# Optimization experiments

Measured on AMD Instinct MI355X. Metric: run time of the kernel, lower is better.

The kernel has to match this reference:

```python
import jax, jax.numpy as jnp
import numpy as np

TAU = 2.0
V_TH = 1.0
ATAN_ALPHA = 2.0
LN_EPS = 1e-5

# Surrogate-gradient spike: forward = Heaviside(v - v_th), backward = ATan surrogate
@jax.custom_vjp
def atan_spike(x):
    return (x >= 0.0).astype(x.dtype)

def _atan_spike_fwd(x):
    return atan_spike(x), x

def _atan_spike_bwd(x, g):
    grad = ATAN_ALPHA / (2.0 * (1.0 + (jnp.pi / 2.0 * ATAN_ALPHA * x) ** 2))
    return (g * grad,)

atan_spike.defvjp(_atan_spike_fwd, _atan_spike_bwd)

def layernorm(x, g, b):
    m = jnp.mean(x, axis=-1, keepdims=True)
    v = jnp.mean((x - m) ** 2, axis=-1, keepdims=True)
    return (x - m) * jax.lax.rsqrt(v + LN_EPS) * g + b

def lif_multistep(x_btd):
    """spikingjelly LIFNode: decay_input=True, v_reset=0.0 (hard reset), detach_reset=True.
    x_btd: [B, T, D]; scan over T with membrane state [B, D]; returns spikes [B, T, D]."""
    x_tbd = jnp.swapaxes(x_btd, 0, 1)  # [T, B, D]
    def step(v, xt):
        h = v + (xt - v) / TAU                      # charge (decay_input, v_reset=0)
        s = atan_spike(h - V_TH)                    # fire
        v_new = h * (1.0 - jax.lax.stop_gradient(s))  # hard reset to 0, detached spike
        return v_new, s
    _, spikes = jax.lax.scan(step, jnp.zeros_like(x_tbd[0]), x_tbd)
    return jnp.swapaxes(spikes, 0, 1)  # [B, T, D]

def setup_inputs() -> dict:
    key = jax.random.key(0)
    ks = jax.random.split(key, 3)
    B, T, D, H = 256, 256, 128, 256
    x = jax.random.normal(ks[0], (B, T, D), dtype=jnp.float32)
    W1 = jax.random.normal(ks[1], (H, D), dtype=jnp.float32) * (1.0 / np.sqrt(D))
    b1 = jnp.zeros((H,), jnp.float32)
    g1 = jnp.ones((H,), jnp.float32)
    be1 = jnp.zeros((H,), jnp.float32)
    W2 = jax.random.normal(ks[2], (D, H), dtype=jnp.float32) * (1.0 / np.sqrt(H))
    b2 = jnp.zeros((D,), jnp.float32)
    g2 = jnp.ones((D,), jnp.float32)
    be2 = jnp.zeros((D,), jnp.float32)
    return {"x": x, "W1": W1, "b1": b1, "g1": g1, "be1": be1,
            "W2": W2, "b2": b2, "g2": g2, "be2": be2}

def reference(x, W1, b1, g1, be1, W2, b2, g2, be2):
    residual = x
    h = jnp.einsum("btd,hd->bth", x, W1) + b1
    h = layernorm(h, g1, be1)
    h = lif_multistep(h)            # dropout is identity at eval
    o = jnp.einsum("bth,dh->btd", h, W2) + b2
    o = layernorm(o, g2, be2)
    o = lif_multistep(o)
    return residual + o
```

## Files before the change

kernel.cpp:

```cpp
#include <hip/hip_runtime.h>
#include <hip/hip_bf16.h>
#include <stdint.h>

#define B_ 256
#define T_ 256
#define D_ 128
#define H_ 256
#define LN_EPS 1e-5

typedef double f64x4 __attribute__((ext_vector_type(4)));

__device__ __forceinline__ bool probe_f64_mfma_layout(int l16, int lg, int* rowp)
{
  const f64x4 zz = {0.0, 0.0, 0.0, 0.0};
  const double pa_r = (lg == 0) ? (double)l16 : 0.0;
  const double pb_1 = (lg == 0) ? 1.0 : 0.0;
  const f64x4 prow = __builtin_amdgcn_mfma_f64_16x16x4f64(pa_r, pb_1, zz, 0, 0, 0);
  const double pa_1 = (lg == 0) ? 1.0 : 0.0;
  const double pb_c = (lg == 0) ? (double)l16 : 0.0;
  const f64x4 pcol = __builtin_amdgcn_mfma_f64_16x16x4f64(pa_1, pb_c, zz, 0, 0, 0);
  bool ok = true;
  int rm = 0, rp = 0;
  #pragma unroll
  for (int r = 0; r < 4; ++r) {
    const int ri = (int)prow[r];
    const int ci = (int)pcol[r];
    rowp[r] = ri;
    ok = ok && ((double)ri == prow[r]) && (ri >= 0) && (ri < 16);
    ok = ok && ((double)ci == pcol[r]) && (ci == l16);
    rm |= 1 << ri;
    rp |= ri << (4 * r);
  }
  ok = ok && (__popc(rm) == 4);
  #pragma unroll
  for (int m = 1; m <= 8; m <<= 1)
    ok = ok && (__shfl_xor(rp, m, 64) == rp);
  int rmw = rm;
  rmw |= __shfl_xor(rmw, 16, 64);
  rmw |= __shfl_xor(rmw, 32, 64);
  ok = ok && (rmw == 0xFFFF);
  return __all((int)ok) != 0;
}

__global__ __launch_bounds__(256, 2) void k1_gemm_ln(
    const float* __restrict__ x, const float* __restrict__ W1,
    const float* __restrict__ b1, const float* __restrict__ g1, const float* __restrict__ be1,
    double* __restrict__ h1, int row0)
{
  __shared__ double As[16 * 66];
  __shared__ double Bs[16 * 258];
  const int tid  = threadIdx.x;
  const int lane = tid & 63, wave = tid >> 6;
  const int l16  = lane & 15, lg = lane >> 4;
  const int orow = blockIdx.x * 64;
  const int grow = row0 + orow;
  const int wrow = wave * 16;

  int rowp[4];
  const bool ok = probe_f64_mfma_layout(l16, lg, rowp);

  auto stage = [&](int kt) {
    __syncthreads();
    {
      const int row = tid >> 2, ko = (tid & 3) * 4;
      const float4 f = *(const float4*)(x + (size_t)(grow + row) * 128 + kt + ko);
      As[(ko+0)*66 + row] = (double)f.x;
      As[(ko+1)*66 + row] = (double)f.y;
      As[(ko+2)*66 + row] = (double)f.z;
      As[(ko+3)*66 + row] = (double)f.w;
    }
    {
      const float* src = W1 + (size_t)tid * 128 + kt;
      #pragma unroll
      for (int j = 0; j < 4; ++j) {
        const float4 f = *(const float4*)(src + j * 4);
        Bs[(j*4+0)*258 + tid] = (double)f.x;
        Bs[(j*4+1)*258 + tid] = (double)f.y;
        Bs[(j*4+2)*258 + tid] = (double)f.z;
        Bs[(j*4+3)*258 + tid] = (double)f.w;
      }
    }
    __syncthreads();
  };

  if (ok) {
    f64x4 acc[16];
    #pragma unroll
    for (int ct = 0; ct < 16; ++ct) acc[ct] = (f64x4){0.0, 0.0, 0.0, 0.0};
    for (int kt = 0; kt < 128; kt += 16) {
      stage(kt);
      #pragma unroll
      for (int ks = 0; ks < 4; ++ks) {
        const int k = ks * 4 + lg;
        const double a = As[k*66 + wrow + l16];
        #pragma unroll
        for (int ct = 0; ct < 16; ++ct) {
          const double b = Bs[k*258 + ct*16 + l16];
          acc[ct] = __builtin_amdgcn_mfma_f64_16x16x4f64(a, b, acc[ct], 0, 0, 0);
        }
      }
    }
    double bb[16];
    #pragma unroll
    for (int ct = 0; ct < 16; ++ct) bb[ct] = (double)b1[ct*16 + l16];
    #pragma unroll
    for (int r = 0; r < 4; ++r) {
      double s = 0.0, q = 0.0;
      #pragma unroll
      for (int ct = 0; ct < 16; ++ct) {
        const double v = acc[ct][r] + bb[ct];
        s += v; q += v * v;
      }
      s += __shfl_xor(s, 1, 64); q += __shfl_xor(q, 1, 64);
      s += __shfl_xor(s, 2, 64); q += __shfl_xor(q, 2, 64);
      s += __shfl_xor(s, 4, 64); q += __shfl_xor(q, 4, 64);
      s += __shfl_xor(s, 8, 64); q += __shfl_xor(q, 8, 64);
      const double mean = s * (1.0/256.0);
      const double var  = q * (1.0/256.0) - mean*mean;
      const double rstd = 1.0 / sqrt(var + LN_EPS);
      const int row = orow + wrow + rowp[r];
      #pragma unroll
      for (int ct = 0; ct < 16; ++ct) {
        const int col = ct*16 + l16;
        const double v = acc[ct][r] + bb[ct];
        h1[(size_t)row*256 + col] = (v - mean) * rstd * (double)g1[col] + (double)be1[col];
      }
    }
  } else {
    double accv[64];
    #pragma unroll
    for (int c = 0; c < 64; ++c) accv[c] = 0.0;
    for (int kt = 0; kt < 128; kt += 16) {
      stage(kt);
      for (int k = 0; k < 16; ++k) {
        const double a = As[k*66 + wrow + l16];
        #pragma unroll
        for (int c = 0; c < 64; ++c)
          accv[c] = fma(a, Bs[k*258 + lg*64 + c], accv[c]);
      }
    }
    double s = 0.0, q = 0.0;
    #pragma unroll
    for (int c = 0; c < 64; ++c) {
      accv[c] += (double)b1[lg*64 + c];
      s += accv[c]; q += accv[c]*accv[c];
    }
    s += __shfl_xor(s, 16, 64); q += __shfl_xor(q, 16, 64);
    s += __shfl_xor(s, 32, 64); q += __shfl_xor(q, 32, 64);
    const double mean = s * (1.0/256.0);
    const double var  = q * (1.0/256.0) - mean*mean;
    const double rstd = 1.0 / sqrt(var + LN_EPS);
    const int row = orow + wrow + l16;
    #pragma unroll
    for (int c = 0; c < 64; ++c) {
      const int col = lg*64 + c;
      h1[(size_t)row*256 + col] = (accv[c] - mean) * rstd * (double)g1[col] + (double)be1[col];
    }
  }
}

__global__ __launch_bounds__(256) void k2_lif(
    const double* __restrict__ h1, uint8_t* __restrict__ s1)
{
  const int ci = blockIdx.x * 256 + threadIdx.x;
  const int b = ci >> 8, h = ci & 255;
  const double* p = h1 + (size_t)b * (T_*H_) + h;
  uint8_t* qp = s1 + (size_t)b * (T_*H_) + h;
  double v = 0.0;
  #pragma unroll 8
  for (int t = 0; t < T_; ++t) {
    const double xv = p[(size_t)t * H_];
    const double hm = v + (xv - v) * 0.5;
    const bool s = (hm >= 1.0);
    v = s ? 0.0 : hm;
    qp[(size_t)t * H_] = s ? (uint8_t)1 : (uint8_t)0;
  }
}

__global__ __launch_bounds__(256, 2) void k3_gemm_ln(
    const uint8_t* __restrict__ s1, const float* __restrict__ W2,
    const float* __restrict__ b2, const float* __restrict__ g2, const float* __restrict__ be2,
    double* __restrict__ h2)
{
  __shared__ double As[16 * 66];
  __shared__ double Bs[16 * 130];
  const int tid  = threadIdx.x;
  const int lane = tid & 63, wave = tid >> 6;
  const int l16  = lane & 15, lg = lane >> 4;
  const int orow = blockIdx.x * 64;
  const int wrow = wave * 16;

  int rowp[4];
  const bool ok = probe_f64_mfma_layout(l16, lg, rowp);

  auto stage = [&](int kt) {
    __syncthreads();
    {
      const int row = tid >> 2, ko = (tid & 3) * 4;
      const uint32_t u = *(const uint32_t*)(s1 + (size_t)(orow + row) * 256 + kt + ko);
      As[(ko+0)*66 + row] = (double)( u        & 0xffu);
      As[(ko+1)*66 + row] = (double)((u >> 8)  & 0xffu);
      As[(ko+2)*66 + row] = (double)((u >> 16) & 0xffu);
      As[(ko+3)*66 + row] = (double)((u >> 24) & 0xffu);
    }
    {
      const int col = tid >> 1, k0 = (tid & 1) * 8;
      const float* src = W2 + (size_t)col * 256 + kt + k0;
      #pragma unroll
      for (int j = 0; j < 2; ++j) {
        const float4 f = *(const float4*)(src + j * 4);
        Bs[(k0+j*4+0)*130 + col] = (double)f.x;
        Bs[(k0+j*4+1)*130 + col] = (double)f.y;
        Bs[(k0+j*4+2)*130 + col] = (double)f.z;
        Bs[(k0+j*4+3)*130 + col] = (double)f.w;
      }
    }
    __syncthreads();
  };

  if (ok) {
    f64x4 acc[8];
    #pragma unroll
    for (int ct = 0; ct < 8; ++ct) acc[ct] = (f64x4){0.0, 0.0, 0.0, 0.0};
    for (int kt = 0; kt < 256; kt += 16) {
      stage(kt);
      #pragma unroll
      for (int ks = 0; ks < 4; ++ks) {
        const int k = ks * 4 + lg;
        const double a = As[k*66 + wrow + l16];
        #pragma unroll
        for (int ct = 0; ct < 8; ++ct) {
          const double b = Bs[k*130 + ct*16 + l16];
          acc[ct] = __builtin_amdgcn_mfma_f64_16x16x4f64(a, b, acc[ct], 0, 0, 0);
        }
      }
    }
    double bb[8];
    #pragma unroll
    for (int ct = 0; ct < 8; ++ct) bb[ct] = (double)b2[ct*16 + l16];
    #pragma unroll
    for (int r = 0; r < 4; ++r) {
      double s = 0.0, q = 0.0;
      #pragma unroll
      for (int ct = 0; ct < 8; ++ct) {
        const double v = acc[ct][r] + bb[ct];
        s += v; q += v * v;
      }
      s += __shfl_xor(s, 1, 64); q += __shfl_xor(q, 1, 64);
      s += __shfl_xor(s, 2, 64); q += __shfl_xor(q, 2, 64);
      s += __shfl_xor(s, 4, 64); q += __shfl_xor(q, 4, 64);
      s += __shfl_xor(s, 8, 64); q += __shfl_xor(q, 8, 64);
      const double mean = s * (1.0/128.0);
      const double var  = q * (1.0/128.0) - mean*mean;
      const double rstd = 1.0 / sqrt(var + LN_EPS);
      const int row = orow + wrow + rowp[r];
      #pragma unroll
      for (int ct = 0; ct < 8; ++ct) {
        const int col = ct*16 + l16;
        const double v = acc[ct][r] + bb[ct];
        h2[(size_t)row*128 + col] = (v - mean) * rstd * (double)g2[col] + (double)be2[col];
      }
    }
  } else {
    double accv[32];
    #pragma unroll
    for (int c = 0; c < 32; ++c) accv[c] = 0.0;
    for (int kt = 0; kt < 256; kt += 16) {
      stage(kt);
      for (int k = 0; k < 16; ++k) {
        const double a = As[k*66 + wrow + l16];
        #pragma unroll
        for (int c = 0; c < 32; ++c)
          accv[c] = fma(a, Bs[k*130 + lg*32 + c], accv[c]);
      }
    }
    double s = 0.0, q = 0.0;
    #pragma unroll
    for (int c = 0; c < 32; ++c) {
      accv[c] += (double)b2[lg*32 + c];
      s += accv[c]; q += accv[c]*accv[c];
    }
    s += __shfl_xor(s, 16, 64); q += __shfl_xor(q, 16, 64);
    s += __shfl_xor(s, 32, 64); q += __shfl_xor(q, 32, 64);
    const double mean = s * (1.0/128.0);
    const double var  = q * (1.0/128.0) - mean*mean;
    const double rstd = 1.0 / sqrt(var + LN_EPS);
    const int row = orow + wrow + l16;
    #pragma unroll
    for (int c = 0; c < 32; ++c) {
      const int col = lg*32 + c;
      h2[(size_t)row*128 + col] = (accv[c] - mean) * rstd * (double)g2[col] + (double)be2[col];
    }
  }
}

__global__ __launch_bounds__(64) void k4_lif_res(
    const double* __restrict__ h2, const float* __restrict__ x,
    float* __restrict__ out, int row0)
{
  const int ci = blockIdx.x * 64 + threadIdx.x;
  const int b = ci >> 7, d = ci & 127;
  const double* p = h2 + (size_t)b * (T_*D_) + d;
  const size_t gbase = ((size_t)row0 + (size_t)b * T_) * D_ + d;
  double v = 0.0;
  #pragma unroll 8
  for (int t = 0; t < T_; ++t) {
    const double hv = p[(size_t)t * D_];
    const double hm = v + (hv - v) * 0.5;
    const bool s = (hm >= 1.0);
    v = s ? 0.0 : hm;
    out[gbase + (size_t)t * D_] = x[gbase + (size_t)t * D_] + (s ? 1.0f : 0.0f);
  }
}

extern "C" void kernel_launch(void* const* d_in, const int* in_sizes, int n_in,
                              void* d_out, int out_size, void* d_ws, size_t ws_size,
                              hipStream_t stream)
{
  const float* x   = (const float*)d_in[0];
  const float* W1  = (const float*)d_in[1];
  const float* b1  = (const float*)d_in[2];
  const float* g1  = (const float*)d_in[3];
  const float* be1 = (const float*)d_in[4];
  const float* W2  = (const float*)d_in[5];
  const float* b2  = (const float*)d_in[6];
  const float* g2  = (const float*)d_in[7];
  const float* be2 = (const float*)d_in[8];
  float* out = (float*)d_out;

  const size_t per_b = (size_t)T_*H_*sizeof(double) + (size_t)T_*H_ + (size_t)T_*D_*sizeof(double);
  int Bc = B_;
  while (Bc > 1 && (size_t)Bc * per_b > ws_size) Bc >>= 1;

  double*  h1 = (double*)d_ws;
  uint8_t* s1 = (uint8_t*)d_ws + (size_t)Bc*T_*H_*sizeof(double);
  double*  h2 = (double*)((uint8_t*)d_ws + (size_t)Bc*T_*H_*sizeof(double) + (size_t)Bc*T_*H_);

  const int nchunk = B_ / Bc;
  for (int c = 0; c < nchunk; ++c) {
    const int row0 = c * Bc * T_;
    k1_gemm_ln<<<dim3(Bc*4), dim3(256), 0, stream>>>(x, W1, b1, g1, be1, h1, row0);
    k2_lif   <<<dim3(Bc),   dim3(256), 0, stream>>>(h1, s1);
    k3_gemm_ln<<<dim3(Bc*4), dim3(256), 0, stream>>>(s1, W2, b2, g2, be2, h2);
    k4_lif_res<<<dim3(Bc*2), dim3(64),  0, stream>>>(h2, x, out, row0);
  }
}
```

Baseline: 309.9 us.

## Prefetch GEMM tiles into registers, swizzle LDS layout, batch LIF scan loads

Both GEMM+LayerNorm kernels now load the next K-tile from global memory into registers while MFMAs run on the current tile. Tiles are stored in a row-major LDS layout with an XOR swizzle and vectorized double2 accesses, and the MFMA-support check becomes a single block-wide flag. The LIF kernels batch 16 timestep loads before the sequential recurrence to expose memory-level parallelism, and k4 moves to 256-thread blocks. The cost is extra registers for the prefetch buffers and the 16-element load arrays, which may lower occupancy.

```diff
diff --git a/kernel.cpp b/kernel.cpp
--- a/kernel.cpp
+++ b/kernel.cpp
@@ -9,6 +9,9 @@
 #define LN_EPS 1e-5
 
 typedef double f64x4 __attribute__((ext_vector_type(4)));
+
+#define LSTRIDE 18
+__device__ __forceinline__ int swz_off(int row, int g) { return row * LSTRIDE + ((g ^ (row & 3)) << 2); }
 
 __device__ __forceinline__ bool probe_f64_mfma_layout(int l16, int lg, int* rowp)
 {
@@ -47,8 +50,9 @@
     const float* __restrict__ b1, const float* __restrict__ g1, const float* __restrict__ be1,
     double* __restrict__ h1, int row0)
 {
-  __shared__ double As[16 * 66];
-  __shared__ double Bs[16 * 258];
+  __shared__ double As[64 * LSTRIDE];
+  __shared__ double Bs[256 * LSTRIDE];
+  __shared__ int ok_sh;
   const int tid  = threadIdx.x;
   const int lane = tid & 63, wave = tid >> 6;
   const int l16  = lane & 15, lg = lane >> 4;
@@ -57,52 +61,120 @@
   const int wrow = wave * 16;
 
   int rowp[4];
-  const bool ok = probe_f64_mfma_layout(l16, lg, rowp);
-
-  auto stage = [&](int kt) {
+  const bool okw = probe_f64_mfma_layout(l16, lg, rowp);
+  if (tid == 0) ok_sh = 1;
+  __syncthreads();
+  if (lane == 0 && !okw) ok_sh = 0;
+  __syncthreads();
+  const bool okb = (ok_sh != 0);
+
+  const int arow = tid >> 2, ag = tid & 3;
+  const float* xsrc = x + (size_t)(grow + arow) * 128 + ag * 4;
+  const float* wsrc = W1 + (size_t)tid * 128;
+
+  float4 xa, wb0, wb1, wb2, wb3;
+  xa  = *(const float4*)(xsrc);
+  wb0 = *(const float4*)(wsrc + 0);
+  wb1 = *(const float4*)(wsrc + 4);
+  wb2 = *(const float4*)(wsrc + 8);
+  wb3 = *(const float4*)(wsrc + 12);
+  {
+    double2* da = (double2*)&As[swz_off(arow, ag)];
+    da[0] = make_double2((double)xa.x, (double)xa.y);
+    da[1] = make_double2((double)xa.z, (double)xa.w);
+    double2* db;
+    db = (double2*)&Bs[swz_off(tid, 0)];
+    db[0] = make_double2((double)wb0.x, (double)wb0.y);
+    db[1] = make_double2((double)wb0.z, (double)wb0.w);
+    db = (double2*)&Bs[swz_off(tid, 1)];
+    db[0] = make_double2((double)wb1.x, (double)wb1.y);
+    db[1] = make_double2((double)wb1.z, (double)wb1.w);
+    db = (double2*)&Bs[swz_off(tid, 2)];
+    db[0] = make_double2((double)wb2.x, (double)wb2.y);
+    db[1] = make_double2((double)wb2.z, (double)wb2.w);
+    db = (double2*)&Bs[swz_off(tid, 3)];
+    db[0] = make_double2((double)wb3.x, (double)wb3.y);
+    db[1] = make_double2((double)wb3.z, (double)wb3.w);
+  }
+  __syncthreads();
+
+  f64x4 acc[16];
+  #pragma unroll
+  for (int ct = 0; ct < 16; ++ct) acc[ct] = (f64x4){0.0, 0.0, 0.0, 0.0};
+  double accv[64];
+  if (!okb) {
+    #pragma unroll
+    for (int c = 0; c < 64; ++c) accv[c] = 0.0;
+  }
+
+  const int vfr = swz_off(wrow + l16, lg);
+  for (int it = 0; it < 8; ++it) {
+    if (it < 7) {
+      const int kt = (it + 1) * 16;
+      xa  = *(const float4*)(xsrc + kt);
+      wb0 = *(const float4*)(wsrc + kt + 0);
+      wb1 = *(const float4*)(wsrc + kt + 4);
+      wb2 = *(const float4*)(wsrc + kt + 8);
+      wb3 = *(const float4*)(wsrc + kt + 12);
+    }
+    if (okb) {
+      const double2* pa = (const double2*)&As[vfr];
+      const double2 a01 = pa[0], a23 = pa[1];
+      double aval[4] = {a01.x, a01.y, a23.x, a23.y};
+      #pragma unroll
+      for (int ctg = 0; ctg < 4; ++ctg) {
+        double bval[4][4];
+        #pragma unroll
+        for (int u = 0; u < 4; ++u) {
+          const int col = (ctg * 4 + u) * 16 + l16;
+          const double2* pb = (const double2*)&Bs[col * LSTRIDE + ((lg ^ (l16 & 3)) << 2)];
+          const double2 b01 = pb[0], b23 = pb[1];
+          bval[u][0] = b01.x; bval[u][1] = b01.y; bval[u][2] = b23.x; bval[u][3] = b23.y;
+        }
+        #pragma unroll
+        for (int ks = 0; ks < 4; ++ks)
+          #pragma unroll
+          for (int u = 0; u < 4; ++u)
+            acc[ctg * 4 + u] = __builtin_amdgcn_mfma_f64_16x16x4f64(
+                aval[ks], bval[u][ks], acc[ctg * 4 + u], 0, 0, 0);
+      }
+    } else {
+      for (int k = 0; k < 16; ++k) {
+        const int rr = wrow + l16;
+        const double a = As[rr * LSTRIDE + ((((k >> 2) ^ (rr & 3)) << 2)) + (k & 3)];
+        #pragma unroll
+        for (int c = 0; c < 64; ++c) {
+          const int col = lg * 64 + c;
+          accv[c] = fma(a, Bs[col * LSTRIDE + ((((k >> 2) ^ (col & 3)) << 2)) + (k & 3)], accv[c]);
+        }
+      }
+    }
     __syncthreads();
-    {
-      const int row = tid >> 2, ko = (tid & 3) * 4;
-      const float4 f = *(const float4*)(x + (size_t)(grow + row) * 128 + kt + ko);
-      As[(ko+0)*66 + row] = (double)f.x;
-      As[(ko+1)*66 + row] = (double)f.y;
-      As[(ko+2)*66 + row] = (double)f.z;
-      As[(ko+3)*66 + row] = (double)f.w;
-    }
-    {
-      const float* src = W1 + (size_t)tid * 128 + kt;
-      #pragma unroll
-      for (int j = 0; j < 4; ++j) {
-        const float4 f = *(const float4*)(src + j * 4);
-        Bs[(j*4+0)*258 + tid] = (double)f.x;
-        Bs[(j*4+1)*258 + tid] = (double)f.y;
-        Bs[(j*4+2)*258 + tid] = (double)f.z;
-        Bs[(j*4+3)*258 + tid] = (double)f.w;
-      }
+    if (it < 7) {
+      double2* da = (double2*)&As[swz_off(arow, ag)];
+      da[0] = make_double2((double)xa.x, (double)xa.y);
+      da[1] = make_double2((double)xa.z, (double)xa.w);
+      double2* db;
+      db = (double2*)&Bs[swz_off(tid, 0)];
+      db[0] = make_double2((double)wb0.x, (double)wb0.y);
+      db[1] = make_double2((double)wb0.z, (double)wb0.w);
+      db = (double2*)&Bs[swz_off(tid, 1)];
+      db[0] = make_double2((double)wb1.x, (double)wb1.y);
+      db[1] = make_double2((double)wb1.z, (double)wb1.w);
+      db = (double2*)&Bs[swz_off(tid, 2)];
+      db[0] = make_double2((double)wb2.x, (double)wb2.y);
+      db[1] = make_double2((double)wb2.z, (double)wb2.w);
+      db = (double2*)&Bs[swz_off(tid, 3)];
+      db[0] = make_double2((double)wb3.x, (double)wb3.y);
+      db[1] = make_double2((double)wb3.z, (double)wb3.w);
     }
     __syncthreads();
-  };
-
-  if (ok) {
-    f64x4 acc[16];
-    #pragma unroll
-    for (int ct = 0; ct < 16; ++ct) acc[ct] = (f64x4){0.0, 0.0, 0.0, 0.0};
-    for (int kt = 0; kt < 128; kt += 16) {
-      stage(kt);
-      #pragma unroll
-      for (int ks = 0; ks < 4; ++ks) {
-        const int k = ks * 4 + lg;
-        const double a = As[k*66 + wrow + l16];
-        #pragma unroll
-        for (int ct = 0; ct < 16; ++ct) {
-          const double b = Bs[k*258 + ct*16 + l16];
-          acc[ct] = __builtin_amdgcn_mfma_f64_16x16x4f64(a, b, acc[ct], 0, 0, 0);
-        }
-      }
-    }
+  }
+
+  if (okb) {
     double bb[16];
     #pragma unroll
-    for (int ct = 0; ct < 16; ++ct) bb[ct] = (double)b1[ct*16 + l16];
+    for (int ct = 0; ct < 16; ++ct) bb[ct] = (double)b1[ct * 16 + l16];
     #pragma unroll
     for (int r = 0; r < 4; ++r) {
       double s = 0.0, q = 0.0;
@@ -115,46 +187,34 @@
       s += __shfl_xor(s, 2, 64); q += __shfl_xor(q, 2, 64);
       s += __shfl_xor(s, 4, 64); q += __shfl_xor(q, 4, 64);
       s += __shfl_xor(s, 8, 64); q += __shfl_xor(q, 8, 64);
-      const double mean = s * (1.0/256.0);
-      const double var  = q * (1.0/256.0) - mean*mean;
+      const double mean = s * (1.0 / 256.0);
+      const double var  = q * (1.0 / 256.0) - mean * mean;
       const double rstd = 1.0 / sqrt(var + LN_EPS);
       const int row = orow + wrow + rowp[r];
       #pragma unroll
       for (int ct = 0; ct < 16; ++ct) {
-        const int col = ct*16 + l16;
+        const int col = ct * 16 + l16;
         const double v = acc[ct][r] + bb[ct];
-        h1[(size_t)row*256 + col] = (v - mean) * rstd * (double)g1[col] + (double)be1[col];
+        h1[(size_t)row * 256 + col] = (v - mean) * rstd * (double)g1[col] + (double)be1[col];
       }
     }
   } else {
-    double accv[64];
-    #pragma unroll
-    for (int c = 0; c < 64; ++c) accv[c] = 0.0;
-    for (int kt = 0; kt < 128; kt += 16) {
-      stage(kt);
-      for (int k = 0; k < 16; ++k) {
-        const double a = As[k*66 + wrow + l16];
-        #pragma unroll
-        for (int c = 0; c < 64; ++c)
-          accv[c] = fma(a, Bs[k*258 + lg*64 + c], accv[c]);
-      }
-    }
     double s = 0.0, q = 0.0;
     #pragma unroll
     for (int c = 0; c < 64; ++c) {
-      accv[c] += (double)b1[lg*64 + c];
-      s += accv[c]; q += accv[c]*accv[c];
+      accv[c] += (double)b1[lg * 64 + c];
+      s += accv[c]; q += accv[c] * accv[c];
     }
     s += __shfl_xor(s, 16, 64); q += __shfl_xor(q, 16, 64);
     s += __shfl_xor(s, 32, 64); q += __shfl_xor(q, 32, 64);
-    const double mean = s * (1.0/256.0);
-    const double var  = q * (1.0/256.0) - mean*mean;
+    const double mean = s * (1.0 / 256.0);
+    const double var  = q * (1.0 / 256.0) - mean * mean;
     const double rstd = 1.0 / sqrt(var + LN_EPS);
     const int row = orow + wrow + l16;
     #pragma unroll
     for (int c = 0; c < 64; ++c) {
-      const int col = lg*64 + c;
-      h1[(size_t)row*256 + col] = (accv[c] - mean) * rstd * (double)g1[col] + (double)be1[col];
+      const int col = lg * 64 + c;
+      h1[(size_t)row * 256 + col] = (accv[c] - mean) * rstd * (double)g1[col] + (double)be1[col];
     }
   }
 }
@@ -164,16 +224,20 @@
 {
   const int ci = blockIdx.x * 256 + threadIdx.x;
   const int b = ci >> 8, h = ci & 255;
-  const double* p = h1 + (size_t)b * (T_*H_) + h;
-  uint8_t* qp = s1 + (size_t)b * (T_*H_) + h;
+  const double* p = h1 + (size_t)b * (T_ * H_) + h;
+  uint8_t* qp = s1 + (size_t)b * (T_ * H_) + h;
   double v = 0.0;
-  #pragma unroll 8
-  for (int t = 0; t < T_; ++t) {
-    const double xv = p[(size_t)t * H_];
-    const double hm = v + (xv - v) * 0.5;
-    const bool s = (hm >= 1.0);
-    v = s ? 0.0 : hm;
-    qp[(size_t)t * H_] = s ? (uint8_t)1 : (uint8_t)0;
+  for (int t0 = 0; t0 < T_; t0 += 16) {
+    double xv[16];
+    #pragma unroll
+    for (int i = 0; i < 16; ++i) xv[i] = p[(size_t)(t0 + i) * H_];
+    #pragma unroll
+    for (int i = 0; i < 16; ++i) {
+      const double hm = v + (xv[i] - v) * 0.5;
+      const bool s = (hm >= 1.0);
+      v = s ? 0.0 : hm;
+      qp[(size_t)(t0 + i) * H_] = s ? (uint8_t)1 : (uint8_t)0;
+    }
   }
 }
 
@@ -182,8 +246,9 @@
     const float* __restrict__ b2, const float* __restrict__ g2, const float* __restrict__ be2,
     double* __restrict__ h2)
 {
-  __shared__ double As[16 * 66];
-  __shared__ double Bs[16 * 130];
+  __shared__ double As[64 * LSTRIDE];
+  __shared__ double Bs[128 * LSTRIDE];
+  __shared__ int ok_sh;
   const int tid  = threadIdx.x;
   const int lane = tid & 63, wave = tid >> 6;
   const int l16  = lane & 15, lg = lane >> 4;
@@ -191,53 +256,106 @@
   const int wrow = wave * 16;
 
   int rowp[4];
-  const bool ok = probe_f64_mfma_layout(l16, lg, rowp);
-
-  auto stage = [&](int kt) {
+  const bool okw = probe_f64_mfma_layout(l16, lg, rowp);
+  if (tid == 0) ok_sh = 1;
+  __syncthreads();
+  if (lane == 0 && !okw) ok_sh = 0;
+  __syncthreads();
+  const bool okb = (ok_sh != 0);
+
+  const int arow = tid >> 2, ag = tid & 3;
+  const int bcol = tid >> 1, bhalf = tid & 1;
+  const uint8_t* asrc = s1 + (size_t)(orow + arow) * 256 + ag * 4;
+  const float* wsrc = W2 + (size_t)bcol * 256 + bhalf * 8;
+
+  uint32_t ua;
+  float4 wb0, wb1;
+  ua  = *(const uint32_t*)(asrc);
+  wb0 = *(const float4*)(wsrc + 0);
+  wb1 = *(const float4*)(wsrc + 4);
+  {
+    double2* da = (double2*)&As[swz_off(arow, ag)];
+    da[0] = make_double2((double)(ua & 0xffu), (double)((ua >> 8) & 0xffu));
+    da[1] = make_double2((double)((ua >> 16) & 0xffu), (double)((ua >> 24) & 0xffu));
+    double2* db;
+    db = (double2*)&Bs[swz_off(bcol, bhalf * 2 + 0)];
+    db[0] = make_double2((double)wb0.x, (double)wb0.y);
+    db[1] = make_double2((double)wb0.z, (double)wb0.w);
+    db = (double2*)&Bs[swz_off(bcol, bhalf * 2 + 1)];
+    db[0] = make_double2((double)wb1.x, (double)wb1.y);
+    db[1] = make_double2((double)wb1.z, (double)wb1.w);
+  }
+  __syncthreads();
+
+  f64x4 acc[8];
+  #pragma unroll
+  for (int ct = 0; ct < 8; ++ct) acc[ct] = (f64x4){0.0, 0.0, 0.0, 0.0};
+  double accv[32];
+  if (!okb) {
+    #pragma unroll
+    for (int c = 0; c < 32; ++c) accv[c] = 0.0;
+  }
+
+  const int vfr = swz_off(wrow + l16, lg);
+  for (int it = 0; it < 16; ++it) {
+    if (it < 15) {
+      const int kt = (it + 1) * 16;
+      ua  = *(const uint32_t*)(asrc + kt);
+      wb0 = *(const float4*)(wsrc + kt + 0);
+      wb1 = *(const float4*)(wsrc + kt + 4);
+    }
+    if (okb) {
+      const double2* pa = (const double2*)&As[vfr];
+      const double2 a01 = pa[0], a23 = pa[1];
+      double aval[4] = {a01.x, a01.y, a23.x, a23.y};
+      #pragma unroll
+      for (int ctg = 0; ctg < 2; ++ctg) {
+        double bval[4][4];
+        #pragma unroll
+        for (int u = 0; u < 4; ++u) {
+          const int col = (ctg * 4 + u) * 16 + l16;
+          const double2* pb = (const double2*)&Bs[col * LSTRIDE + ((lg ^ (l16 & 3)) << 2)];
+          const double2 b01 = pb[0], b23 = pb[1];
+          bval[u][0] = b01.x; bval[u][1] = b01.y; bval[u][2] = b23.x; bval[u][3] = b23.y;
+        }
+        #pragma unroll
+        for (int ks = 0; ks < 4; ++ks)
+          #pragma unroll
+          for (int u = 0; u < 4; ++u)
+            acc[ctg * 4 + u] = __builtin_amdgcn_mfma_f64_16x16x4f64(
+                aval[ks], bval[u][ks], acc[ctg * 4 + u], 0, 0, 0);
+      }
+    } else {
+      for (int k = 0; k < 16; ++k) {
+        const int rr = wrow + l16;
+        const double a = As[rr * LSTRIDE + ((((k >> 2) ^ (rr & 3)) << 2)) + (k & 3)];
+        #pragma unroll
+        for (int c = 0; c < 32; ++c) {
+          const int col = lg * 32 + c;
+          accv[c] = fma(a, Bs[col * LSTRIDE + ((((k >> 2) ^ (col & 3)) << 2)) + (k & 3)], accv[c]);
+        }
+      }
+    }
     __syncthreads();
-    {
-      const int row = tid >> 2, ko = (tid & 3) * 4;
-      const uint32_t u = *(const uint32_t*)(s1 + (size_t)(orow + row) * 256 + kt + ko);
-      As[(ko+0)*66 + row] = (double)( u        & 0xffu);
-      As[(ko+1)*66 + row] = (double)((u >> 8)  & 0xffu);
-      As[(ko+2)*66 + row] = (double)((u >> 16) & 0xffu);
-      As[(ko+3)*66 + row] = (double)((u >> 24) & 0xffu);
-    }
-    {
-      const int col = tid >> 1, k0 = (tid & 1) * 8;
-      const float* src = W2 + (size_t)col * 256 + kt + k0;
-      #pragma unroll
-      for (int j = 0; j < 2; ++j) {
-        const float4 f = *(const float4*)(src + j * 4);
-        Bs[(k0+j*4+0)*130 + col] = (double)f.x;
-        Bs[(k0+j*4+1)*130 + col] = (double)f.y;
-        Bs[(k0+j*4+2)*130 + col] = (double)f.z;
-        Bs[(k0+j*4+3)*130 + col] = (double)f.w;
-      }
+    if (it < 15) {
+      double2* da = (double2*)&As[swz_off(arow, ag)];
+      da[0] = make_double2((double)(ua & 0xffu), (double)((ua >> 8) & 0xffu));
+      da[1] = make_double2((double)((ua >> 16) & 0xffu), (double)((ua >> 24) & 0xffu));
+      double2* db;
+      db = (double2*)&Bs[swz_off(bcol, bhalf * 2 + 0)];
+      db[0] = make_double2((double)wb0.x, (double)wb0.y);
+      db[1] = make_double2((double)wb0.z, (double)wb0.w);
+      db = (double2*)&Bs[swz_off(bcol, bhalf * 2 + 1)];
+      db[0] = make_double2((double)wb1.x, (double)wb1.y);
+      db[1] = make_double2((double)wb1.z, (double)wb1.w);
     }
     __syncthreads();
-  };
-
-  if (ok) {
-    f64x4 acc[8];
-    #pragma unroll
-    for (int ct = 0; ct < 8; ++ct) acc[ct] = (f64x4){0.0, 0.0, 0.0, 0.0};
-    for (int kt = 0; kt < 256; kt += 16) {
-      stage(kt);
-      #pragma unroll
-      for (int ks = 0; ks < 4; ++ks) {
-        const int k = ks * 4 + lg;
-        const double a = As[k*66 + wrow + l16];
-        #pragma unroll
-        for (int ct = 0; ct < 8; ++ct) {
-          const double b = Bs[k*130 + ct*16 + l16];
-          acc[ct] = __builtin_amdgcn_mfma_f64_16x16x4f64(a, b, acc[ct], 0, 0, 0);
-        }
-      }
-    }
+  }
+
+  if (okb) {
     double bb[8];
     #pragma unroll
-    for (int ct = 0; ct < 8; ++ct) bb[ct] = (double)b2[ct*16 + l16];
+    for (int ct = 0; ct < 8; ++ct) bb[ct] = (double)b2[ct * 16 + l16];
     #pragma unroll
     for (int r = 0; r < 4; ++r) {
       double s = 0.0, q = 0.0;
@@ -250,66 +368,62 @@
       s += __shfl_xor(s, 2, 64); q += __shfl_xor(q, 2, 64);
       s += __shfl_xor(s, 4, 64); q += __shfl_xor(q, 4, 64);
       s += __shfl_xor(s, 8, 64); q += __shfl_xor(q, 8, 64);
-      const double mean = s * (1.0/128.0);
-      const double var  = q * (1.0/128.0) - mean*mean;
+      const double mean = s * (1.0 / 128.0);
+      const double var  = q * (1.0 / 128.0) - mean * mean;
       const double rstd = 1.0 / sqrt(var + LN_EPS);
       const int row = orow + wrow + rowp[r];
       #pragma unroll
       for (int ct = 0; ct < 8; ++ct) {
-        const int col = ct*16 + l16;
+        const int col = ct * 16 + l16;
         const double v = acc[ct][r] + bb[ct];
-        h2[(size_t)row*128 + col] = (v - mean) * rstd * (double)g2[col] + (double)be2[col];
+        h2[(size_t)row * 128 + col] = (v - mean) * rstd * (double)g2[col] + (double)be2[col];
       }
     }
   } else {
-    double accv[32];
-    #pragma unroll
-    for (int c = 0; c < 32; ++c) accv[c] = 0.0;
-    for (int kt = 0; kt < 256; kt += 16) {
-      stage(kt);
-      for (int k = 0; k < 16; ++k) {
-        const double a = As[k*66 + wrow + l16];
-        #pragma unroll
-        for (int c = 0; c < 32; ++c)
-          accv[c] = fma(a, Bs[k*130 + lg*32 + c], accv[c]);
-      }
-    }
     double s = 0.0, q = 0.0;
     #pragma unroll
     for (int c = 0; c < 32; ++c) {
-      accv[c] += (double)b2[lg*32 + c];
-      s += accv[c]; q += accv[c]*accv[c];
+      accv[c] += (double)b2[lg * 32 + c];
+      s += accv[c]; q += accv[c] * accv[c];
     }
     s += __shfl_xor(s, 16, 64); q += __shfl_xor(q, 16, 64);
     s += __shfl_xor(s, 32, 64); q += __shfl_xor(q, 32, 64);
-    const double mean = s * (1.0/128.0);
-    const double var  = q * (1.0/128.0) - mean*mean;
+    const double mean = s * (1.0 / 128.0);
+    const double var  = q * (1.0 / 128.0) - mean * mean;
     const double rstd = 1.0 / sqrt(var + LN_EPS);
     const int row = orow + wrow + l16;
     #pragma unroll
     for (int c = 0; c < 32; ++c) {
-      const int col = lg*32 + c;
-      h2[(size_t)row*128 + col] = (accv[c] - mean) * rstd * (double)g2[col] + (double)be2[col];
-    }
-  }
-}
-
-__global__ __launch_bounds__(64) void k4_lif_res(
+      const int col = lg * 32 + c;
+      h2[(size_t)row * 128 + col] = (accv[c] - mean) * rstd * (double)g2[col] + (double)be2[col];
+    }
+  }
+}
+
+__global__ __launch_bounds__(256) void k4_lif_res(
     const double* __restrict__ h2, const float* __restrict__ x,
-    float* __restrict__ out, int row0)
-{
-  const int ci = blockIdx.x * 64 + threadIdx.x;
+    float* __restrict__ out, int row0, int nch)
+{
+  const int ci = blockIdx.x * 256 + threadIdx.x;
+  if (ci >= nch) return;
   const int b = ci >> 7, d = ci & 127;
-  const double* p = h2 + (size_t)b * (T_*D_) + d;
+  const double* p = h2 + (size_t)b * (T_ * D_) + d;
   const size_t gbase = ((size_t)row0 + (size_t)b * T_) * D_ + d;
   double v = 0.0;
-  #pragma unroll 8
-  for (int t = 0; t < T_; ++t) {
-    const double hv = p[(size_t)t * D_];
-    const double hm = v + (hv - v) * 0.5;
-    const bool s = (hm >= 1.0);
-    v = s ? 0.0 : hm;
-    out[gbase + (size_t)t * D_] = x[gbase + (size_t)t * D_] + (s ? 1.0f : 0.0f);
+  for (int t0 = 0; t0 < T_; t0 += 16) {
+    double hv[16];
+    float xr[16];
+    #pragma unroll
+    for (int i = 0; i < 16; ++i) hv[i] = p[(size_t)(t0 + i) * D_];
+    #pragma unroll
+    for (int i = 0; i < 16; ++i) xr[i] = x[gbase + (size_t)(t0 + i) * D_];
+    #pragma unroll
+    for (int i = 0; i < 16; ++i) {
+      const double hm = v + (hv[i] - v) * 0.5;
+      const bool s = (hm >= 1.0);
+      v = s ? 0.0 : hm;
+      out[gbase + (size_t)(t0 + i) * D_] = xr[i] + (s ? 1.0f : 0.0f);
+    }
   }
 }
 
@@ -337,11 +451,13 @@
   double*  h2 = (double*)((uint8_t*)d_ws + (size_t)Bc*T_*H_*sizeof(double) + (size_t)Bc*T_*H_);
 
   const int nchunk = B_ / Bc;
+  const int nch4 = Bc * D_;
+  const int g4 = (nch4 + 255) / 256;
   for (int c = 0; c < nchunk; ++c) {
     const int row0 = c * Bc * T_;
     k1_gemm_ln<<<dim3(Bc*4), dim3(256), 0, stream>>>(x, W1, b1, g1, be1, h1, row0);
     k2_lif   <<<dim3(Bc),   dim3(256), 0, stream>>>(h1, s1);
     k3_gemm_ln<<<dim3(Bc*4), dim3(256), 0, stream>>>(s1, W2, b2, g2, be2, h2);
-    k4_lif_res<<<dim3(Bc*2), dim3(64),  0, stream>>>(h2, x, out, row0);
-  }
-}
+    k4_lif_res<<<dim3(g4),  dim3(256), 0, stream>>>(h2, x, out, row0, nch4);
+  }
+}
```

Measured after the change: 794.5 us. 2.56x slower.
